# Kernel optimization log

Measured on AMD Instinct MI355X. Metric: run time of the kernel, lower is better.

The kernel has to match this reference:

```python
import jax, jax.numpy as jnp
import numpy as np
from jax import lax


def _attention_conv(x, Wq, bq, Wk, bk, Wv, bv, head_w, p):
    # x: [B,C,H,W]; Wq/Wk/Wv: [heads, D, D] (torch Linear weight, out x in); b*: [heads, D]
    B, C, H, W = x.shape
    pad_h = (p * (1 + H // p) - H) % p
    pad_w = (p * (1 + W // p) - W) % p
    xp = jnp.pad(x, ((0, 0), (0, 0), (p + pad_h, p), (p + pad_w, p)), mode='reflect')
    num_h = (H + pad_h) // p
    num_w = (W + pad_w) // p
    # view padded image as a grid of (num_h+2) x (num_w+2) patches of size p x p
    g = xp.reshape(B, C, num_h + 2, p, num_w + 2, p)
    # 9-patch neighborhood per window (equivalent to unfold with window=3p, stride=p)
    nb = jnp.stack([g[:, :, di:di + num_h, :, dj:dj + num_w, :]
                    for di in range(3) for dj in range(3)], axis=2)  # [B,C,9,num_h,p,num_w,p]
    tokens = nb.transpose(0, 3, 5, 2, 1, 4, 6).reshape(B * num_h * num_w, 9, C * p * p)
    D = C * p * p
    q = jnp.einsum('npd,hed->nhpe', tokens, Wq) + bq[None, :, None, :]
    k = jnp.einsum('npd,hed->nhpe', tokens, Wk) + bk[None, :, None, :]
    v = jnp.einsum('npd,hed->nhpe', tokens, Wv) + bv[None, :, None, :]
    # core patch (index 4 = center of 3x3) attends to all 9 patches
    score = jnp.einsum('nhe,nhpe->nhp', q[:, :, 4, :], k) / jnp.sqrt(jnp.float32(D))
    attn = jax.nn.softmax(score, axis=-1)               # [N,heads,9]
    out = jnp.einsum('nhp,nhpe->nhe', attn, v)          # [N,heads,D]
    mixed = jnp.einsum('h,nhe->ne', head_w[0], out)     # head-weight mixing -> [N,D]
    out = mixed.reshape(B, num_h, num_w, C, p, p).transpose(0, 3, 1, 4, 2, 5)
    out = out.reshape(B, C, num_h * p, num_w * p)
    return out[:, :, pad_h:, pad_w:]


def _dehaze(x, p3, p6, p9, conv0_w, conv0_b):
    b, c, h, w = x.shape
    avg = jnp.mean((1.0 - x).reshape(b, c, -1), axis=-1, keepdims=True)  # [b,c,1]
    xg1 = jax.nn.softmax(avg, axis=-1)[..., None]                        # softmax over size-1 dim -> ones
    xg = jnp.max((x * xg1).reshape(b, 1, -1), axis=-1, keepdims=True)[..., None]  # [b,1,1,1]
    x3 = _attention_conv(x, *p3, 1)
    x6 = _attention_conv(x3, *p6, 2)
    x9 = _attention_conv(x6, *p9, 3)
    cat = jnp.concatenate([x9, x6, x3], axis=1)
    x0 = jax.nn.relu(lax.conv_general_dilated(cat, conv0_w, (1, 1), [(2, 2), (2, 2)])
                     + conv0_b[None, :, None, None])
    return jax.nn.relu(x * x0 + (xg - x0))


def setup_inputs() -> dict:
    key = jax.random.key(0)
    ks = jax.random.split(key, 12)
    inp = {'x': jax.random.uniform(ks[0], (2, 3, 384, 384), jnp.float32)}
    specs = [('3', 6, 3), ('6', 4, 12), ('9', 2, 27)]  # (stage, num_heads, D=C*p*p)
    i = 1
    for name, h, d in specs:
        for proj in ('q', 'k', 'v'):
            inp['w%s_%s' % (name, proj)] = jax.random.normal(ks[i], (h, d, d), jnp.float32) * 0.02
            inp['b%s_%s' % (name, proj)] = jnp.zeros((h, d), jnp.float32)
            i += 1
        inp['hw%s' % name] = jnp.ones((1, h), jnp.float32) / h
    inp['conv0_w'] = jax.random.normal(ks[10], (3, 9, 5, 5), jnp.float32) * 0.02
    inp['conv0_b'] = jnp.zeros((3,), jnp.float32)
    return inp


def reference(x, w3_q, b3_q, w3_k, b3_k, w3_v, b3_v, hw3,
              w6_q, b6_q, w6_k, b6_k, w6_v, b6_v, hw6,
              w9_q, b9_q, w9_k, b9_k, w9_v, b9_v, hw9,
              conv0_w, conv0_b):
    p3 = (w3_q, b3_q, w3_k, b3_k, w3_v, b3_v, hw3)
    p6 = (w6_q, b6_q, w6_k, b6_k, w6_v, b6_v, hw6)
    p9 = (w9_q, b9_q, w9_k, b9_k, w9_v, b9_v, hw9)
    return _dehaze(x, p3, p6, p9, conv0_w, conv0_b)
```

## Files before the change

kernel.cpp:

```cpp
#include <hip/hip_runtime.h>

#define HH 384
#define HWPX (HH*HH)

#define WOFF3 16
#define HS3   40
#define WOFF6 256
#define HS6   328
#define WOFF9 1568
#define HS9   1600
#define CATOFF 8192
#define P9BOFF (CATOFF + 2*9*HWPX)
#define WS_NEED ((size_t)(P9BOFF + 2*3*HWPX) * 4)

__device__ __forceinline__ float4 fma4s(float4 a, float4 w, float t) {
    a.x += w.x * t; a.y += w.y * t; a.z += w.z * t; a.w += w.w * t; return a;
}
__device__ __forceinline__ float dot4(float4 a, float4 b) {
    return a.x * b.x + a.y * b.y + a.z * b.z + a.w * b.w;
}

__global__ __launch_bounds__(256) void pre_xg(
    const float* __restrict__ w3q, const float* __restrict__ b3q,
    const float* __restrict__ w3k, const float* __restrict__ b3k,
    const float* __restrict__ w3v, const float* __restrict__ b3v, const float* __restrict__ hw3,
    const float* __restrict__ w6q, const float* __restrict__ b6q,
    const float* __restrict__ w6k, const float* __restrict__ b6k,
    const float* __restrict__ w6v, const float* __restrict__ b6v, const float* __restrict__ hw6,
    const float* __restrict__ w9q, const float* __restrict__ b9q,
    const float* __restrict__ w9k, const float* __restrict__ b9k,
    const float* __restrict__ w9v, const float* __restrict__ b9v, const float* __restrict__ hw9,
    const float* __restrict__ x, float* __restrict__ ws)
{
    __shared__ float sm[4];
    const int blk = blockIdx.x;
    const int tid = threadIdx.x;

    if (blk < 12) {
        int stage = blk < 6 ? 0 : (blk < 10 ? 1 : 2);
        int h = blk - (stage == 0 ? 0 : (stage == 1 ? 6 : 10));
        const float* WQ[3] = {w3q, w6q, w9q};
        const float* BQ[3] = {b3q, b6q, b9q};
        const float* WK[3] = {w3k, w6k, w9k};
        const float* BK[3] = {b3k, b6k, b9k};
        const float* WV_[3] = {w3v, w6v, w9v};
        const float* BV[3] = {b3v, b6v, b9v};
        const float* HWp[3] = {hw3, hw6, hw9};
        const int Ds[3] = {3, 12, 27};
        const int DPs[3] = {4, 12, 28};
        const int WOFFs[3] = {WOFF3, WOFF6, WOFF9};
        const int HSs[3] = {HS3, HS6, HS9};

        const int D = Ds[stage], DP = DPs[stage];
        const float* wq = WQ[stage] + h * D * D;
        const float* bq = BQ[stage] + h * D;
        const float* wk = WK[stage] + h * D * D;
        const float* bk = BK[stage] + h * D;
        const float* wv = WV_[stage] + h * D * D;
        const float* bv = BV[stage] + h * D;
        const float hwv = HWp[stage][h];
        float* base = ws + WOFFs[stage] + h * HSs[stage];
        const float scale = rsqrtf((float)D);

        for (int i = tid; i < D * DP; i += 256) {
            int a = i / DP, b = i % DP;
            float m = 0.f;
            if (b < D) for (int e = 0; e < D; ++e) m += wk[e * D + b] * wq[e * D + a];
            base[i] = scale * m;
            float wvv = 0.f;
            if (b < D) wvv = hwv * wv[a * D + b];
            base[D * DP + i] = wvv;
        }
        for (int i = tid; i < DP; i += 256) {
            float cv = 0.f, uv = 0.f;
            if (i < D) for (int e = 0; e < D; ++e) {
                cv += bq[e] * wk[e * D + i];
                uv += wq[e * D + i] * bk[e];
            }
            base[2 * D * DP + i] = scale * cv;
            base[2 * D * DP + DP + i] = scale * uv;
            base[2 * D * DP + 2 * DP + i] = (i < D) ? hwv * bv[i] : 0.f;
        }
        if (tid == 0) {
            float s = 0.f;
            for (int e = 0; e < D; ++e) s += bq[e] * bk[e];
            base[2 * D * DP + 3 * DP] = scale * s;
        }
    } else {
        int i2 = blk - 12;
        int b = i2 / 144, chunk = i2 % 144;
        const float4* xb = (const float4*)(x + (size_t)b * 3 * HWPX + chunk * 3072);
        float m = 0.f;
        for (int j = tid; j < 768; j += 256) {
            float4 v = xb[j];
            m = fmaxf(m, fmaxf(fmaxf(v.x, v.y), fmaxf(v.z, v.w)));
        }
        for (int off = 32; off; off >>= 1)
            m = fmaxf(m, __shfl_down(m, off));
        if ((tid & 63) == 0) sm[tid >> 6] = m;
        __syncthreads();
        if (tid == 0) {
            float mm = fmaxf(fmaxf(sm[0], sm[1]), fmaxf(sm[2], sm[3]));
            atomicMax((int*)&ws[b], __float_as_int(mm));
        }
    }
}

template <int P, int HEADS, int HSPLIT>
__global__ __launch_bounds__(256) void attn_cell(
    const float* __restrict__ in, long in_bstride,
    float* __restrict__ outA, long outA_bstride,
    float* __restrict__ outB, long outB_bstride,
    const float* __restrict__ wsw)
{
    constexpr int C = 3, D = C * P * P, DP = (D + 3) & ~3, NREG = DP / 4;
    constexpr int HS = 2 * D * DP + 3 * DP + 4;
    constexpr int HPT = HEADS / HSPLIT;
    __shared__ __align__(16) float scell[324 * DP];
    __shared__ __align__(16) float sw[HPT * HS];

    const int tid = threadIdx.x;
    const int z = blockIdx.z;
    const int b = z & 1;
    const int hs = z >> 1;
    const int BWY = blockIdx.y * 16, BWX = blockIdx.x * 16;

    const float* inb = in + (size_t)b * in_bstride;
    constexpr int XW = 18 * P;
    constexpr int TOT = 3 * P * 18 * XW;
    for (int i = tid; i < TOT; i += 256) {
        int c = i / (P * 18 * XW);
        int rem = i % (P * 18 * XW);
        int r = rem / (18 * XW);
        int rem2 = rem % (18 * XW);
        int cy = rem2 / XW, xx = rem2 % XW;
        int y = (BWY + cy) * P + r - P; y = y < 0 ? -y : (y >= HH ? 2 * HH - 2 - y : y);
        int x = BWX * P + xx - P;       x = x < 0 ? -x : (x >= HH ? 2 * HH - 2 - x : x);
        int cx = xx / P, s = xx % P;
        scell[(cy * 18 + cx) * DP + (c * P + r) * P + s] = inb[c * HWPX + y * HH + x];
    }
    if constexpr (DP > D) {
        for (int j = tid; j < 324; j += 256) scell[j * DP + D] = 0.f;
    }
    const float* wsrc = wsw + (size_t)hs * HPT * HS;
    for (int i = tid; i < HPT * HS; i += 256) sw[i] = wsrc[i];
    __syncthreads();

    const int wx = tid & 15, wy = tid >> 4;

    float t4[DP];
    {
        const float4* T4p = (const float4*)&scell[((wy + 1) * 18 + wx + 1) * DP];
#pragma unroll
        for (int k = 0; k < NREG; ++k) {
            float4 v = T4p[k];
            t4[4 * k] = v.x; t4[4 * k + 1] = v.y; t4[4 * k + 2] = v.z; t4[4 * k + 3] = v.w;
        }
    }
    float mixed[D];
#pragma unroll
    for (int e = 0; e < D; ++e) mixed[e] = 0.f;

#pragma unroll 1
    for (int hh = 0; hh < HPT; ++hh) {
        const float* hb = sw + hh * HS;
        const float* ccb = hb + 2 * D * DP;
        float4 qk[NREG];
        {
            const float4* cp = (const float4*)ccb;
#pragma unroll
            for (int k = 0; k < NREG; ++k) qk[k] = cp[k];
        }
        float su = ccb[3 * DP];
#pragma unroll
        for (int a = 0; a < D; ++a) {
            const float t = t4[a];
            su += ccb[DP + a] * t;
            const float4* Mr = (const float4*)(hb + a * DP);
#pragma unroll
            for (int k = 0; k < NREG; ++k) qk[k] = fma4s(qk[k], Mr[k], t);
        }
        float denom = 0.f;
        float4 wt[NREG];
#pragma unroll
        for (int k = 0; k < NREG; ++k) wt[k] = make_float4(0.f, 0.f, 0.f, 0.f);
#pragma unroll
        for (int di = 0; di < 3; ++di)
#pragma unroll
            for (int dj = 0; dj < 3; ++dj) {
                const float4* cp = (const float4*)&scell[((wy + di) * 18 + wx + dj) * DP];
                float4 cv[NREG];
#pragma unroll
                for (int k = 0; k < NREG; ++k) cv[k] = cp[k];
                float s = su;
#pragma unroll
                for (int k = 0; k < NREG; ++k) s += dot4(qk[k], cv[k]);
                const float e = __expf(s);
                denom += e;
#pragma unroll
                for (int k = 0; k < NREG; ++k) wt[k] = fma4s(wt[k], cv[k], e);
            }
        const float winv = 1.f / denom;
#pragma unroll
        for (int k = 0; k < NREG; ++k) {
            wt[k].x *= winv; wt[k].y *= winv; wt[k].z *= winv; wt[k].w *= winv;
        }
        const float* WVb = hb + D * DP;
#pragma unroll
        for (int e = 0; e < D; ++e) {
            const float4* Wr = (const float4*)(WVb + e * DP);
            float o = ccb[2 * DP + e];
#pragma unroll
            for (int k = 0; k < NREG; ++k) o += dot4(Wr[k], wt[k]);
            mixed[e] += o;
        }
    }

    float* outp = (hs == 0) ? (outA + (size_t)b * outA_bstride)
                            : (outB + (size_t)b * outB_bstride);
#pragma unroll
    for (int c = 0; c < C; ++c)
#pragma unroll
        for (int r = 0; r < P; ++r)
#pragma unroll
            for (int s = 0; s < P; ++s)
                outp[c * HWPX + ((BWY + wy) * P + r) * HH + (BWX + wx) * P + s] =
                    mixed[(c * P + r) * P + s];
}

__global__ __launch_bounds__(128) void conv_final(
    const float* __restrict__ cat, const float* __restrict__ p9b, int addp9,
    const float* __restrict__ w, const float* __restrict__ bias,
    const float* __restrict__ x, const float* __restrict__ xg,
    float* __restrict__ out)
{
    __shared__ float tile[9][20][40];
    const int tid = threadIdx.x;
    const int b = blockIdx.z;
    const int bx = blockIdx.x * 32, by = blockIdx.y * 16;
    const float* catb = cat + (size_t)b * 9 * HWPX;
    const float* p9bb = p9b + (size_t)b * 3 * HWPX;

    for (int i = tid; i < 9 * 20 * 10; i += 128) {
        int ci = i / 200;
        int rem = i % 200;
        int row = rem / 10, c4 = rem % 10;
        int y = by + row - 2, xx = bx - 4 + 4 * c4;
        float4 v = {0.f, 0.f, 0.f, 0.f};
        if (y >= 0 && y < HH && xx >= 0 && xx <= HH - 4) {
            v = *(const float4*)&catb[ci * HWPX + y * HH + xx];
            if (addp9 && ci < 3) {
                float4 u = *(const float4*)&p9bb[ci * HWPX + y * HH + xx];
                v.x += u.x; v.y += u.y; v.z += u.z; v.w += u.w;
            }
        }
        *(float4*)&tile[ci][row][4 * c4] = v;
    }
    __syncthreads();

    const int tx = tid & 7, ty = tid >> 3;
    float acc0[4], acc1[4], acc2[4];
    const float b0 = bias[0], b1 = bias[1], b2 = bias[2];
#pragma unroll
    for (int j = 0; j < 4; ++j) { acc0[j] = b0; acc1[j] = b1; acc2[j] = b2; }

#pragma unroll
    for (int ky = 0; ky < 5; ++ky) {
#pragma unroll 1
        for (int ci = 0; ci < 9; ++ci) {
            const float4 ra = *(const float4*)&tile[ci][ty + ky][4 * tx];
            const float4 rb = *(const float4*)&tile[ci][ty + ky][4 * tx + 4];
            const float4 rc = *(const float4*)&tile[ci][ty + ky][4 * tx + 8];
            const float r[12] = {ra.x, ra.y, ra.z, ra.w, rb.x, rb.y, rb.z, rb.w,
                                 rc.x, rc.y, rc.z, rc.w};
            const float* __restrict__ w0 = w + (0 * 9 + ci) * 25 + ky * 5;
            const float* __restrict__ w1 = w + (1 * 9 + ci) * 25 + ky * 5;
            const float* __restrict__ w2 = w + (2 * 9 + ci) * 25 + ky * 5;
#pragma unroll
            for (int j = 0; j < 4; ++j)
#pragma unroll
                for (int kx = 0; kx < 5; ++kx) {
                    const float t = r[j + kx + 2];
                    acc0[j] += t * w0[kx];
                    acc1[j] += t * w1[kx];
                    acc2[j] += t * w2[kx];
                }
        }
    }

    const int yb = by + ty, xb = bx + 4 * tx;
    const float xgv = xg[b];
    float* accs[3] = {acc0, acc1, acc2};
#pragma unroll
    for (int co = 0; co < 3; ++co) {
        const float4 xv = *(const float4*)&x[((size_t)(b * 3 + co)) * HWPX + yb * HH + xb];
        const float* a = accs[co];
        float4 ov;
        float x0;
        x0 = fmaxf(a[0], 0.f); ov.x = fmaxf(xv.x * x0 + xgv - x0, 0.f);
        x0 = fmaxf(a[1], 0.f); ov.y = fmaxf(xv.y * x0 + xgv - x0, 0.f);
        x0 = fmaxf(a[2], 0.f); ov.z = fmaxf(xv.z * x0 + xgv - x0, 0.f);
        x0 = fmaxf(a[3], 0.f); ov.w = fmaxf(xv.w * x0 + xgv - x0, 0.f);
        *(float4*)&out[((size_t)(b * 3 + co)) * HWPX + yb * HH + xb] = ov;
    }
}

extern "C" void kernel_launch(void* const* d_in, const int* in_sizes, int n_in,
                              void* d_out, int out_size, void* d_ws, size_t ws_size,
                              hipStream_t stream) {
    const float* x   = (const float*)d_in[0];
    const float* w3q = (const float*)d_in[1];
    const float* b3q = (const float*)d_in[2];
    const float* w3k = (const float*)d_in[3];
    const float* b3k = (const float*)d_in[4];
    const float* w3v = (const float*)d_in[5];
    const float* b3v = (const float*)d_in[6];
    const float* hw3 = (const float*)d_in[7];
    const float* w6q = (const float*)d_in[8];
    const float* b6q = (const float*)d_in[9];
    const float* w6k = (const float*)d_in[10];
    const float* b6k = (const float*)d_in[11];
    const float* w6v = (const float*)d_in[12];
    const float* b6v = (const float*)d_in[13];
    const float* hw6 = (const float*)d_in[14];
    const float* w9q = (const float*)d_in[15];
    const float* b9q = (const float*)d_in[16];
    const float* w9k = (const float*)d_in[17];
    const float* b9k = (const float*)d_in[18];
    const float* w9v = (const float*)d_in[19];
    const float* b9v = (const float*)d_in[20];
    const float* hw9 = (const float*)d_in[21];
    const float* c0w = (const float*)d_in[22];
    const float* c0b = (const float*)d_in[23];

    float* out = (float*)d_out;
    float* ws  = (float*)d_ws;
    float* cat = ws + CATOFF;
    float* p9b = ws + P9BOFF;
    const bool split9 = ws_size >= WS_NEED;

    pre_xg<<<300, 256, 0, stream>>>(
        w3q, b3q, w3k, b3k, w3v, b3v, hw3,
        w6q, b6q, w6k, b6k, w6v, b6v, hw6,
        w9q, b9q, w9k, b9k, w9v, b9v, hw9, x, ws);

    attn_cell<1, 6, 1><<<dim3(24, 24, 2), 256, 0, stream>>>(
        x, 3 * HWPX, cat + 6 * HWPX, 9 * HWPX, cat + 6 * HWPX, 9 * HWPX, ws + WOFF3);
    attn_cell<2, 4, 1><<<dim3(12, 12, 2), 256, 0, stream>>>(
        cat + 6 * HWPX, 9 * HWPX, cat + 3 * HWPX, 9 * HWPX, cat + 3 * HWPX, 9 * HWPX, ws + WOFF6);
    if (split9)
        attn_cell<3, 2, 2><<<dim3(8, 8, 4), 256, 0, stream>>>(
            cat + 3 * HWPX, 9 * HWPX, cat, 9 * HWPX, p9b, 3 * HWPX, ws + WOFF9);
    else
        attn_cell<3, 2, 1><<<dim3(8, 8, 2), 256, 0, stream>>>(
            cat + 3 * HWPX, 9 * HWPX, cat, 9 * HWPX, cat, 9 * HWPX, ws + WOFF9);

    conv_final<<<dim3(12, 24, 2), 128, 0, stream>>>(
        cat, p9b, split9 ? 1 : 0, c0w, c0b, x, ws, out);
}
```

Before: 216.5 us.

## Specialize attention kernels per stage with head-parallel threads and smaller blocks

Replaces the templated attention kernel with three hand-specialized kernels. Stage 6 gives each head its own wavefront, and stage 9 splits each window across a 4-thread team with shuffle reductions, reducing per-thread register arrays. Head outputs are summed through shared memory, and the two-buffer head split for stage 9 is removed. The final convolution is restructured to 256 threads with cached weights. Launch counts are higher and smaller tiles mean more redundant halo loads.

```diff
diff --git a/kernel.cpp b/kernel.cpp
--- a/kernel.cpp
+++ b/kernel.cpp
@@ -8,16 +8,21 @@
 #define WOFF6 256
 #define HS6   328
 #define WOFF9 1568
-#define HS9   1600
+#define HS9   1828
 #define CATOFF 8192
-#define P9BOFF (CATOFF + 2*9*HWPX)
-#define WS_NEED ((size_t)(P9BOFF + 2*3*HWPX) * 4)
-
+
+__device__ __forceinline__ int rx(int g) {
+    g = g < 0 ? -g : g;
+    return g >= HH ? 2 * HH - 2 - g : g;
+}
 __device__ __forceinline__ float4 fma4s(float4 a, float4 w, float t) {
     a.x += w.x * t; a.y += w.y * t; a.z += w.z * t; a.w += w.w * t; return a;
 }
 __device__ __forceinline__ float dot4(float4 a, float4 b) {
     return a.x * b.x + a.y * b.y + a.z * b.z + a.w * b.w;
+}
+__device__ __forceinline__ float f4c(const float4& v, int j) {
+    return j == 0 ? v.x : (j == 1 ? v.y : (j == 2 ? v.z : v.w));
 }
 
 __global__ __launch_bounds__(256) void pre_xg(
@@ -47,7 +52,7 @@
         const float* BV[3] = {b3v, b6v, b9v};
         const float* HWp[3] = {hw3, hw6, hw9};
         const int Ds[3] = {3, 12, 27};
-        const int DPs[3] = {4, 12, 28};
+        const int DPs[3] = {4, 12, 32};
         const int WOFFs[3] = {WOFF3, WOFF6, WOFF9};
         const int HSs[3] = {HS3, HS6, HS9};
 
@@ -106,202 +111,298 @@
     }
 }
 
-template <int P, int HEADS, int HSPLIT>
-__global__ __launch_bounds__(256) void attn_cell(
-    const float* __restrict__ in, long in_bstride,
-    float* __restrict__ outA, long outA_bstride,
-    float* __restrict__ outB, long outB_bstride,
+__global__ __launch_bounds__(256) void attn3(
+    const float* __restrict__ in, float* __restrict__ out,
     const float* __restrict__ wsw)
 {
-    constexpr int C = 3, D = C * P * P, DP = (D + 3) & ~3, NREG = DP / 4;
-    constexpr int HS = 2 * D * DP + 3 * DP + 4;
-    constexpr int HPT = HEADS / HSPLIT;
+    constexpr int DP = 4;
     __shared__ __align__(16) float scell[324 * DP];
-    __shared__ __align__(16) float sw[HPT * HS];
+    __shared__ __align__(16) float sw[6 * HS3];
 
     const int tid = threadIdx.x;
-    const int z = blockIdx.z;
-    const int b = z & 1;
-    const int hs = z >> 1;
+    const int b = blockIdx.z;
     const int BWY = blockIdx.y * 16, BWX = blockIdx.x * 16;
-
-    const float* inb = in + (size_t)b * in_bstride;
-    constexpr int XW = 18 * P;
-    constexpr int TOT = 3 * P * 18 * XW;
-    for (int i = tid; i < TOT; i += 256) {
-        int c = i / (P * 18 * XW);
-        int rem = i % (P * 18 * XW);
-        int r = rem / (18 * XW);
-        int rem2 = rem % (18 * XW);
-        int cy = rem2 / XW, xx = rem2 % XW;
-        int y = (BWY + cy) * P + r - P; y = y < 0 ? -y : (y >= HH ? 2 * HH - 2 - y : y);
-        int x = BWX * P + xx - P;       x = x < 0 ? -x : (x >= HH ? 2 * HH - 2 - x : x);
-        int cx = xx / P, s = xx % P;
-        scell[(cy * 18 + cx) * DP + (c * P + r) * P + s] = inb[c * HWPX + y * HH + x];
-    }
-    if constexpr (DP > D) {
-        for (int j = tid; j < 324; j += 256) scell[j * DP + D] = 0.f;
-    }
-    const float* wsrc = wsw + (size_t)hs * HPT * HS;
-    for (int i = tid; i < HPT * HS; i += 256) sw[i] = wsrc[i];
+    const float* inb = in + (size_t)b * 3 * HWPX;
+
+    for (int i = tid; i < 240; i += 256) sw[i] = wsw[i];
+    for (int i = tid; i < 972; i += 256) {
+        int c = i / 324;
+        int rem = i % 324;
+        int cy = rem / 18, cx = rem % 18;
+        int y = rx(BWY + cy - 1);
+        int x = rx(BWX + cx - 1);
+        scell[(cy * 18 + cx) * DP + c] = inb[c * HWPX + y * HH + x];
+    }
+    for (int j = tid; j < 324; j += 256) scell[j * DP + 3] = 0.f;
     __syncthreads();
 
     const int wx = tid & 15, wy = tid >> 4;
-
-    float t4[DP];
-    {
-        const float4* T4p = (const float4*)&scell[((wy + 1) * 18 + wx + 1) * DP];
-#pragma unroll
-        for (int k = 0; k < NREG; ++k) {
-            float4 v = T4p[k];
-            t4[4 * k] = v.x; t4[4 * k + 1] = v.y; t4[4 * k + 2] = v.z; t4[4 * k + 3] = v.w;
-        }
-    }
-    float mixed[D];
-#pragma unroll
-    for (int e = 0; e < D; ++e) mixed[e] = 0.f;
-
+    const float4 t4 = *(const float4*)&scell[((wy + 1) * 18 + wx + 1) * DP];
+
+    float m0 = 0.f, m1 = 0.f, m2 = 0.f;
 #pragma unroll 1
-    for (int hh = 0; hh < HPT; ++hh) {
-        const float* hb = sw + hh * HS;
-        const float* ccb = hb + 2 * D * DP;
-        float4 qk[NREG];
-        {
-            const float4* cp = (const float4*)ccb;
-#pragma unroll
-            for (int k = 0; k < NREG; ++k) qk[k] = cp[k];
-        }
-        float su = ccb[3 * DP];
-#pragma unroll
-        for (int a = 0; a < D; ++a) {
-            const float t = t4[a];
-            su += ccb[DP + a] * t;
-            const float4* Mr = (const float4*)(hb + a * DP);
-#pragma unroll
-            for (int k = 0; k < NREG; ++k) qk[k] = fma4s(qk[k], Mr[k], t);
-        }
-        float denom = 0.f;
-        float4 wt[NREG];
-#pragma unroll
-        for (int k = 0; k < NREG; ++k) wt[k] = make_float4(0.f, 0.f, 0.f, 0.f);
-#pragma unroll
-        for (int di = 0; di < 3; ++di)
-#pragma unroll
-            for (int dj = 0; dj < 3; ++dj) {
-                const float4* cp = (const float4*)&scell[((wy + di) * 18 + wx + dj) * DP];
-                float4 cv[NREG];
-#pragma unroll
-                for (int k = 0; k < NREG; ++k) cv[k] = cp[k];
-                float s = su;
-#pragma unroll
-                for (int k = 0; k < NREG; ++k) s += dot4(qk[k], cv[k]);
-                const float e = __expf(s);
-                denom += e;
-#pragma unroll
-                for (int k = 0; k < NREG; ++k) wt[k] = fma4s(wt[k], cv[k], e);
-            }
-        const float winv = 1.f / denom;
-#pragma unroll
-        for (int k = 0; k < NREG; ++k) {
-            wt[k].x *= winv; wt[k].y *= winv; wt[k].z *= winv; wt[k].w *= winv;
-        }
-        const float* WVb = hb + D * DP;
-#pragma unroll
-        for (int e = 0; e < D; ++e) {
-            const float4* Wr = (const float4*)(WVb + e * DP);
-            float o = ccb[2 * DP + e];
-#pragma unroll
-            for (int k = 0; k < NREG; ++k) o += dot4(Wr[k], wt[k]);
-            mixed[e] += o;
-        }
-    }
-
-    float* outp = (hs == 0) ? (outA + (size_t)b * outA_bstride)
-                            : (outB + (size_t)b * outB_bstride);
-#pragma unroll
-    for (int c = 0; c < C; ++c)
-#pragma unroll
-        for (int r = 0; r < P; ++r)
-#pragma unroll
-            for (int s = 0; s < P; ++s)
-                outp[c * HWPX + ((BWY + wy) * P + r) * HH + (BWX + wx) * P + s] =
-                    mixed[(c * P + r) * P + s];
-}
-
-__global__ __launch_bounds__(128) void conv_final(
-    const float* __restrict__ cat, const float* __restrict__ p9b, int addp9,
-    const float* __restrict__ w, const float* __restrict__ bias,
-    const float* __restrict__ x, const float* __restrict__ xg,
-    float* __restrict__ out)
+    for (int h = 0; h < 6; ++h) {
+        const float* hb = &sw[h * HS3];
+        float4 qk = *(const float4*)(hb + 24);
+        float su = hb[36] + dot4(*(const float4*)(hb + 28), t4);
+        qk = fma4s(qk, *(const float4*)(hb + 0), t4.x);
+        qk = fma4s(qk, *(const float4*)(hb + 4), t4.y);
+        qk = fma4s(qk, *(const float4*)(hb + 8), t4.z);
+        float den = 0.f; float4 wt = {0.f, 0.f, 0.f, 0.f};
+#pragma unroll
+        for (int p = 0; p < 9; ++p) {
+            const int di = p / 3, dj = p % 3;
+            const float4 cv = *(const float4*)&scell[((wy + di) * 18 + wx + dj) * DP];
+            float e = __expf(su + dot4(qk, cv));
+            den += e; wt = fma4s(wt, cv, e);
+        }
+        float wi = 1.f / den;
+        wt.x *= wi; wt.y *= wi; wt.z *= wi; wt.w *= wi;
+        m0 += hb[32] + dot4(*(const float4*)(hb + 12), wt);
+        m1 += hb[33] + dot4(*(const float4*)(hb + 16), wt);
+        m2 += hb[34] + dot4(*(const float4*)(hb + 20), wt);
+    }
+    float* outb = out + (size_t)b * 9 * HWPX;
+    const int gy = BWY + wy, gx = BWX + wx;
+    outb[6 * HWPX + gy * HH + gx] = m0;
+    outb[7 * HWPX + gy * HH + gx] = m1;
+    outb[8 * HWPX + gy * HH + gx] = m2;
+}
+
+__global__ __launch_bounds__(256) void attn6(
+    const float* __restrict__ cat, float* __restrict__ catOut,
+    const float* __restrict__ wsw)
+{
+    __shared__ __align__(16) float scell[1200];
+    __shared__ __align__(16) float sw[1312];
+    __shared__ float comb[3072];
+
+    const int tid = threadIdx.x;
+    const int b = blockIdx.z;
+    const int BCX = blockIdx.x * 8, BCY = blockIdx.y * 8;
+    const float* inb = cat + (size_t)b * 9 * HWPX + 6 * HWPX;
+
+    for (int i = tid; i < 328; i += 256)
+        ((float4*)sw)[i] = ((const float4*)wsw)[i];
+    const int by0 = 2 * BCY - 2, bx0 = 2 * BCX - 2;
+    for (int i = tid; i < 1200; i += 256) {
+        int c = i / 400; int rem = i - c * 400;
+        int row = rem / 20, col = rem % 20;
+        int gy = rx(by0 + row), gx = rx(bx0 + col);
+        scell[((row >> 1) * 10 + (col >> 1)) * 12 + c * 4 + (row & 1) * 2 + (col & 1)]
+            = inb[c * HWPX + gy * HH + gx];
+    }
+    __syncthreads();
+
+    const int h = tid >> 6, w = tid & 63;
+    const int wx = w & 7, wy = w >> 3;
+    const float* hb = &sw[h * HS6];
+
+    const float4* cc4 = (const float4*)&scell[((wy + 1) * 10 + (wx + 1)) * 12];
+    const float4 t40 = cc4[0], t41 = cc4[1], t42 = cc4[2];
+
+    float4 qk0 = *(const float4*)(hb + 288);
+    float4 qk1 = *(const float4*)(hb + 292);
+    float4 qk2 = *(const float4*)(hb + 296);
+    float su = hb[324] + dot4(*(const float4*)(hb + 300), t40)
+             + dot4(*(const float4*)(hb + 304), t41)
+             + dot4(*(const float4*)(hb + 308), t42);
+#pragma unroll
+    for (int a = 0; a < 12; ++a) {
+        const float t = f4c(a < 4 ? t40 : (a < 8 ? t41 : t42), a & 3);
+        const float4* Mr = (const float4*)(hb + 12 * a);
+        qk0 = fma4s(qk0, Mr[0], t);
+        qk1 = fma4s(qk1, Mr[1], t);
+        qk2 = fma4s(qk2, Mr[2], t);
+    }
+    float den = 0.f;
+    float4 wt0 = {0,0,0,0}, wt1 = {0,0,0,0}, wt2 = {0,0,0,0};
+#pragma unroll
+    for (int p = 0; p < 9; ++p) {
+        const int di = p / 3, dj = p % 3;
+        const float4* cp = (const float4*)&scell[((wy + di) * 10 + (wx + dj)) * 12];
+        const float4 c0 = cp[0], c1 = cp[1], c2 = cp[2];
+        float e = __expf(su + dot4(qk0, c0) + dot4(qk1, c1) + dot4(qk2, c2));
+        den += e;
+        wt0 = fma4s(wt0, c0, e);
+        wt1 = fma4s(wt1, c1, e);
+        wt2 = fma4s(wt2, c2, e);
+    }
+    const float wi = 1.f / den;
+    wt0.x *= wi; wt0.y *= wi; wt0.z *= wi; wt0.w *= wi;
+    wt1.x *= wi; wt1.y *= wi; wt1.z *= wi; wt1.w *= wi;
+    wt2.x *= wi; wt2.y *= wi; wt2.z *= wi; wt2.w *= wi;
+
+    float* cbp = &comb[(h * 64 + w) * 12];
+#pragma unroll
+    for (int e = 0; e < 12; ++e) {
+        const float4* Wr = (const float4*)(hb + 144 + 12 * e);
+        cbp[e] = hb[312 + e] + dot4(Wr[0], wt0) + dot4(Wr[1], wt1) + dot4(Wr[2], wt2);
+    }
+    __syncthreads();
+
+    float* outb = catOut + (size_t)b * 9 * HWPX + 3 * HWPX;
+    for (int i = tid; i < 768; i += 256) {
+        int w2 = i / 12, e = i % 12;
+        float v = comb[w2 * 12 + e] + comb[(64 + w2) * 12 + e]
+                + comb[(128 + w2) * 12 + e] + comb[(192 + w2) * 12 + e];
+        int c = e >> 2, r = (e >> 1) & 1, s = e & 1;
+        int gy = 2 * (BCY + (w2 >> 3)) + r, gx = 2 * (BCX + (w2 & 7)) + s;
+        outb[c * HWPX + gy * HH + gx] = v;
+    }
+}
+
+__global__ __launch_bounds__(256) void attn9(
+    const float* __restrict__ cat, float* __restrict__ catOut,
+    const float* __restrict__ wsw)
+{
+    __shared__ __align__(16) float scell[2160];
+    __shared__ __align__(16) float sw[3656];
+    __shared__ float comb[1728];
+
+    const int tid = threadIdx.x;
+    const int b = blockIdx.z;
+    const int BCX = blockIdx.x * 8, BCY = blockIdx.y * 4;
+    const float* inb = cat + (size_t)b * 9 * HWPX + 3 * HWPX;
+
+    for (int i = tid; i < 914; i += 256)
+        ((float4*)sw)[i] = ((const float4*)wsw)[i];
+    const int by0 = 3 * BCY - 3, bx0 = 3 * BCX - 3;
+    for (int i = tid; i < 1620; i += 256) {
+        int c = i / 540; int rem = i - c * 540;
+        int row = rem / 30, col = rem % 30;
+        int gy = rx(by0 + row), gx = rx(bx0 + col);
+        scell[((row / 3) * 10 + (col / 3)) * 36 + c * 9 + (row % 3) * 3 + (col % 3)]
+            = inb[c * HWPX + gy * HH + gx];
+    }
+    for (int i = tid; i < 300; i += 256) scell[(i / 5) * 36 + 27 + (i % 5)] = 0.f;
+    __syncthreads();
+
+    const int t = tid & 3, team = tid >> 2;
+    const int h = team >> 5, w = team & 31;
+    const int wx = w & 7, wy = w >> 3;
+    const int k0 = t, k1 = t + 4;
+    const float* hb = &sw[h * HS9];
+
+    const float4* cc4 = (const float4*)&scell[((wy + 1) * 10 + (wx + 1)) * 36];
+    float4 t4r[8];
+#pragma unroll
+    for (int k = 0; k < 8; ++k) t4r[k] = cc4[k];
+
+    float4 qk0 = *(const float4*)(hb + 1728 + 4 * k0);
+    float4 qk1 = *(const float4*)(hb + 1728 + 4 * k1);
+#pragma unroll
+    for (int a = 0; a < 27; ++a) {
+        const float tv = f4c(t4r[a >> 2], a & 3);
+        qk0 = fma4s(qk0, *(const float4*)(hb + a * 32 + 4 * k0), tv);
+        qk1 = fma4s(qk1, *(const float4*)(hb + a * 32 + 4 * k1), tv);
+    }
+    float upart = dot4(*(const float4*)(hb + 1760 + 4 * k0), cc4[k0])
+                + dot4(*(const float4*)(hb + 1760 + 4 * k1), cc4[k1]);
+    const float s0v = hb[1824];
+
+    float den = 0.f;
+    float4 wt0 = {0,0,0,0}, wt1 = {0,0,0,0};
+#pragma unroll
+    for (int p = 0; p < 9; ++p) {
+        const int di = p / 3, dj = p % 3;
+        const float4* cp = (const float4*)&scell[((wy + di) * 10 + (wx + dj)) * 36];
+        const float4 c0 = cp[k0], c1 = cp[k1];
+        float part = upart + dot4(qk0, c0) + dot4(qk1, c1);
+        part += __shfl_xor(part, 1);
+        part += __shfl_xor(part, 2);
+        const float e = __expf(s0v + part);
+        den += e;
+        wt0 = fma4s(wt0, c0, e);
+        wt1 = fma4s(wt1, c1, e);
+    }
+    const float wi = 1.f / den;
+    wt0.x *= wi; wt0.y *= wi; wt0.z *= wi; wt0.w *= wi;
+    wt1.x *= wi; wt1.y *= wi; wt1.z *= wi; wt1.w *= wi;
+
+    float* cbp = &comb[(h * 32 + w) * 27];
+#pragma unroll
+    for (int e = 0; e < 27; ++e) {
+        float po = dot4(*(const float4*)(hb + 864 + e * 32 + 4 * k0), wt0)
+                 + dot4(*(const float4*)(hb + 864 + e * 32 + 4 * k1), wt1);
+        po += __shfl_xor(po, 1);
+        po += __shfl_xor(po, 2);
+        if (t == 0) cbp[e] = po + hb[1792 + e];
+    }
+    __syncthreads();
+
+    float* outb = catOut + (size_t)b * 9 * HWPX;
+    for (int i = tid; i < 864; i += 256) {
+        int w2 = i / 27, e = i % 27;
+        float v = comb[w2 * 27 + e] + comb[(32 + w2) * 27 + e];
+        int c = e / 9, r = (e % 9) / 3, s = e % 3;
+        int gy = 3 * (BCY + (w2 >> 3)) + r, gx = 3 * (BCX + (w2 & 7)) + s;
+        outb[c * HWPX + gy * HH + gx] = v;
+    }
+}
+
+__global__ __launch_bounds__(256) void conv_final(
+    const float* __restrict__ cat, const float* __restrict__ cw,
+    const float* __restrict__ cb, const float* __restrict__ x,
+    const float* __restrict__ xg, float* __restrict__ out)
 {
     __shared__ float tile[9][20][40];
+    __shared__ float sw[678];
     const int tid = threadIdx.x;
     const int b = blockIdx.z;
     const int bx = blockIdx.x * 32, by = blockIdx.y * 16;
     const float* catb = cat + (size_t)b * 9 * HWPX;
-    const float* p9bb = p9b + (size_t)b * 3 * HWPX;
-
-    for (int i = tid; i < 9 * 20 * 10; i += 128) {
-        int ci = i / 200;
-        int rem = i % 200;
+
+    for (int i = tid; i < 678; i += 256) sw[i] = (i < 675) ? cw[i] : cb[i - 675];
+    for (int i = tid; i < 1800; i += 256) {
+        int ci = i / 200, rem = i % 200;
         int row = rem / 10, c4 = rem % 10;
         int y = by + row - 2, xx = bx - 4 + 4 * c4;
         float4 v = {0.f, 0.f, 0.f, 0.f};
-        if (y >= 0 && y < HH && xx >= 0 && xx <= HH - 4) {
+        if (y >= 0 && y < HH && xx >= 0 && xx <= HH - 4)
             v = *(const float4*)&catb[ci * HWPX + y * HH + xx];
-            if (addp9 && ci < 3) {
-                float4 u = *(const float4*)&p9bb[ci * HWPX + y * HH + xx];
-                v.x += u.x; v.y += u.y; v.z += u.z; v.w += u.w;
+        *(float4*)&tile[ci][row][4 * c4] = v;
+    }
+    __syncthreads();
+
+    const int pxx = tid & 31, py0 = (tid >> 5) * 2;
+    float acc[2][3];
+    acc[0][0] = acc[1][0] = sw[675];
+    acc[0][1] = acc[1][1] = sw[676];
+    acc[0][2] = acc[1][2] = sw[677];
+
+#pragma unroll 1
+    for (int ci = 0; ci < 9; ++ci) {
+        float rv[6][5];
+#pragma unroll
+        for (int rr = 0; rr < 6; ++rr)
+#pragma unroll
+            for (int cc = 0; cc < 5; ++cc)
+                rv[rr][cc] = tile[ci][py0 + rr][pxx + 2 + cc];
+#pragma unroll
+        for (int ky = 0; ky < 5; ++ky)
+#pragma unroll
+            for (int kx = 0; kx < 5; ++kx) {
+                const float w0 = sw[(0 * 9 + ci) * 25 + ky * 5 + kx];
+                const float w1 = sw[(1 * 9 + ci) * 25 + ky * 5 + kx];
+                const float w2 = sw[(2 * 9 + ci) * 25 + ky * 5 + kx];
+                const float ta = rv[ky][kx], tb = rv[ky + 1][kx];
+                acc[0][0] += ta * w0; acc[0][1] += ta * w1; acc[0][2] += ta * w2;
+                acc[1][0] += tb * w0; acc[1][1] += tb * w1; acc[1][2] += tb * w2;
             }
-        }
-        *(float4*)&tile[ci][row][4 * c4] = v;
-    }
-    __syncthreads();
-
-    const int tx = tid & 7, ty = tid >> 3;
-    float acc0[4], acc1[4], acc2[4];
-    const float b0 = bias[0], b1 = bias[1], b2 = bias[2];
-#pragma unroll
-    for (int j = 0; j < 4; ++j) { acc0[j] = b0; acc1[j] = b1; acc2[j] = b2; }
-
-#pragma unroll
-    for (int ky = 0; ky < 5; ++ky) {
-#pragma unroll 1
-        for (int ci = 0; ci < 9; ++ci) {
-            const float4 ra = *(const float4*)&tile[ci][ty + ky][4 * tx];
-            const float4 rb = *(const float4*)&tile[ci][ty + ky][4 * tx + 4];
-            const float4 rc = *(const float4*)&tile[ci][ty + ky][4 * tx + 8];
-            const float r[12] = {ra.x, ra.y, ra.z, ra.w, rb.x, rb.y, rb.z, rb.w,
-                                 rc.x, rc.y, rc.z, rc.w};
-            const float* __restrict__ w0 = w + (0 * 9 + ci) * 25 + ky * 5;
-            const float* __restrict__ w1 = w + (1 * 9 + ci) * 25 + ky * 5;
-            const float* __restrict__ w2 = w + (2 * 9 + ci) * 25 + ky * 5;
-#pragma unroll
-            for (int j = 0; j < 4; ++j)
-#pragma unroll
-                for (int kx = 0; kx < 5; ++kx) {
-                    const float t = r[j + kx + 2];
-                    acc0[j] += t * w0[kx];
-                    acc1[j] += t * w1[kx];
-                    acc2[j] += t * w2[kx];
-                }
-        }
-    }
-
-    const int yb = by + ty, xb = bx + 4 * tx;
+    }
+
     const float xgv = xg[b];
-    float* accs[3] = {acc0, acc1, acc2};
-#pragma unroll
-    for (int co = 0; co < 3; ++co) {
-        const float4 xv = *(const float4*)&x[((size_t)(b * 3 + co)) * HWPX + yb * HH + xb];
-        const float* a = accs[co];
-        float4 ov;
-        float x0;
-        x0 = fmaxf(a[0], 0.f); ov.x = fmaxf(xv.x * x0 + xgv - x0, 0.f);
-        x0 = fmaxf(a[1], 0.f); ov.y = fmaxf(xv.y * x0 + xgv - x0, 0.f);
-        x0 = fmaxf(a[2], 0.f); ov.z = fmaxf(xv.z * x0 + xgv - x0, 0.f);
-        x0 = fmaxf(a[3], 0.f); ov.w = fmaxf(xv.w * x0 + xgv - x0, 0.f);
-        *(float4*)&out[((size_t)(b * 3 + co)) * HWPX + yb * HH + xb] = ov;
+#pragma unroll
+    for (int jj = 0; jj < 2; ++jj) {
+        const int gy = by + py0 + jj, gx = bx + pxx;
+#pragma unroll
+        for (int co = 0; co < 3; ++co) {
+            const float x0 = fmaxf(acc[jj][co], 0.f);
+            const float xv = x[((size_t)(b * 3 + co)) * HWPX + gy * HH + gx];
+            out[((size_t)(b * 3 + co)) * HWPX + gy * HH + gx] =
+                fmaxf(xv * x0 + xgv - x0, 0.f);
+        }
     }
 }
 
@@ -336,25 +437,15 @@
     float* out = (float*)d_out;
     float* ws  = (float*)d_ws;
     float* cat = ws + CATOFF;
-    float* p9b = ws + P9BOFF;
-    const bool split9 = ws_size >= WS_NEED;
 
     pre_xg<<<300, 256, 0, stream>>>(
         w3q, b3q, w3k, b3k, w3v, b3v, hw3,
         w6q, b6q, w6k, b6k, w6v, b6v, hw6,
         w9q, b9q, w9k, b9k, w9v, b9v, hw9, x, ws);
 
-    attn_cell<1, 6, 1><<<dim3(24, 24, 2), 256, 0, stream>>>(
-        x, 3 * HWPX, cat + 6 * HWPX, 9 * HWPX, cat + 6 * HWPX, 9 * HWPX, ws + WOFF3);
-    attn_cell<2, 4, 1><<<dim3(12, 12, 2), 256, 0, stream>>>(
-        cat + 6 * HWPX, 9 * HWPX, cat + 3 * HWPX, 9 * HWPX, cat + 3 * HWPX, 9 * HWPX, ws + WOFF6);
-    if (split9)
-        attn_cell<3, 2, 2><<<dim3(8, 8, 4), 256, 0, stream>>>(
-            cat + 3 * HWPX, 9 * HWPX, cat, 9 * HWPX, p9b, 3 * HWPX, ws + WOFF9);
-    else
-        attn_cell<3, 2, 1><<<dim3(8, 8, 2), 256, 0, stream>>>(
-            cat + 3 * HWPX, 9 * HWPX, cat, 9 * HWPX, cat, 9 * HWPX, ws + WOFF9);
-
-    conv_final<<<dim3(12, 24, 2), 128, 0, stream>>>(
-        cat, p9b, split9 ? 1 : 0, c0w, c0b, x, ws, out);
-}
+    attn3<<<dim3(24, 24, 2), 256, 0, stream>>>(x, cat, ws + WOFF3);
+    attn6<<<dim3(24, 24, 2), 256, 0, stream>>>(cat, cat, ws + WOFF6);
+    attn9<<<dim3(16, 32, 2), 256, 0, stream>>>(cat, cat, ws + WOFF9);
+
+    conv_final<<<dim3(12, 24, 2), 256, 0, stream>>>(cat, c0w, c0b, x, ws, out);
+}
```

Result: faster. 195.7 us (-9.6%).
